# Optimization experiments

Measured on AMD Instinct MI355X. Metric: run time of the kernel, lower is better.

The kernel has to match this reference:

```python
import jax, jax.numpy as jnp
import numpy as np

EPS_POS = 0.65
EPS_NEG = 0.4
TAU = 0.03
TEMPERATURE = 0.07


def setup_inputs() -> dict:
    key = jax.random.key(0)
    k1, k2 = jax.random.split(key)
    N, H, W, C = 256, 14, 14, 512  # ResNet18 layer4 features (448x448 frame), pooled audio
    frame = jax.random.normal(k1, (N, H, W, C), dtype=jnp.float32)
    audio = jax.random.normal(k2, (N, C), dtype=jnp.float32)
    return {"frame": frame, "audio": audio}


def reference(frame, audio):
    # frame: [N, H, W, C] vision backbone features; audio: [N, C] pooled audio embedding
    N = frame.shape[0]
    f = frame * jax.lax.rsqrt(jnp.sum(frame * frame, axis=3, keepdims=True))  # l2_normalize axis=3
    a = audio * jax.lax.rsqrt(jnp.sum(audio * audio, axis=1, keepdims=True))  # l2_normalize axis=1

    # S_ii: per-sample spatial similarity map [N, 1, H, W]
    S_ii = jnp.einsum('nhwc,nc->nhw', f, a)[:, None, :, :]
    # S_ij: cross-batch similarity [N, K, H, W] (K == N)
    S_ij = jnp.einsum('nhwc,kc->nkhw', f, a)

    m_ip = jax.nn.sigmoid((S_ii - EPS_POS) / TAU)   # positive soft-mask
    neg = 1.0 - jax.nn.sigmoid((S_ii - EPS_NEG) / TAU)  # hard-negative soft-mask

    # Pi: masked mean of positive similarities -> [N, 1]
    Pi = jnp.sum(m_ip * S_ii, axis=(2, 3)) / jnp.sum(m_ip, axis=(2, 3))

    n_all = jax.nn.sigmoid((S_ij - EPS_POS) / TAU)
    mask = 1.0 - 100.0 * jnp.eye(N, dtype=frame.dtype)  # kill diagonal (self) pairs
    Ni_easy = (jnp.sum(n_all * S_ij, axis=(2, 3)) / jnp.sum(n_all, axis=(2, 3))) * mask  # [N, N]
    Ni_hard = jnp.sum(neg * S_ii, axis=(2, 3)) / jnp.sum(neg, axis=(2, 3))  # [N, 1]

    data = jnp.concatenate([Pi, Ni_hard, Ni_easy], axis=1) * TEMPERATURE  # [N, N+2]

    # __calc_loss (faithful to TF broadcasting: Pi_d is [N,1], Ni_d is [N] -> [N,N] broadcast)
    Pi_d = data[:, 0:1]
    Ni_d = jnp.sum(data[:, 1:], axis=1)
    Pi_e = jnp.exp(Pi_d)
    Ni_e = jnp.exp(Ni_d)
    loss = (-1.0 / N) * jnp.sum(jnp.log(Pi_e / (Pi_e + Ni_e)))
    return loss
```

## Files before the change

kernel.cpp:

```cpp
#include <hip/hip_runtime.h>
#include <stdint.h>

#define NFR 256
#define HW 196
#define CH 512
#define EPS_POS 0.65f
#define EPS_NEG 0.40f
#define INV_TAU (1.0f/0.03f)
#define TEMP 0.07f

typedef __bf16 bf16x8 __attribute__((ext_vector_type(8)));
typedef float f32x4 __attribute__((ext_vector_type(4)));

typedef const __attribute__((address_space(1))) unsigned int* as1_u32p;
typedef __attribute__((address_space(3))) unsigned int* as3_u32p;
#define GLL(gp, lp) __builtin_amdgcn_global_load_lds((as1_u32p)(const void*)(gp), (as3_u32p)(void*)(lp), 16, 0, 0)

__device__ __forceinline__ float sigmoidf_(float x) {
  return 1.0f / (1.0f + __expf(-x));
}

__device__ __forceinline__ unsigned short f2bf(float x) {
  unsigned int u = __float_as_uint(x);
  unsigned int r = u + 0x7FFFu + ((u >> 16) & 1u);
  return (unsigned short)(r >> 16);
}

__global__ __launch_bounds__(64) void audio_norm_k(const float* __restrict__ audio,
                                                   unsigned short* __restrict__ abf) {
  const int r = blockIdx.x;
  const int l = threadIdx.x;
  const float4* src = reinterpret_cast<const float4*>(audio + (size_t)r * CH);
  float4 a = src[l];
  float4 b = src[64 + l];
  float ss = a.x*a.x + a.y*a.y + a.z*a.z + a.w*a.w
           + b.x*b.x + b.y*b.y + b.z*b.z + b.w*b.w;
#pragma unroll
  for (int m = 1; m < 64; m <<= 1) ss += __shfl_xor(ss, m);
  float sc = rsqrtf(ss);
  ushort4 o;
  o.x = f2bf(a.x*sc); o.y = f2bf(a.y*sc); o.z = f2bf(a.z*sc); o.w = f2bf(a.w*sc);
  reinterpret_cast<ushort4*>(abf + (size_t)r * CH)[l] = o;
  o.x = f2bf(b.x*sc); o.y = f2bf(b.y*sc); o.z = f2bf(b.z*sc); o.w = f2bf(b.w*sc);
  reinterpret_cast<ushort4*>(abf + (size_t)r * CH)[64 + l] = o;
}

__global__ __launch_bounds__(256) void frame_norm_k(const float* __restrict__ frame,
                                                    unsigned short* __restrict__ fbf) {
  const int w = threadIdx.x >> 6;
  const int l = threadIdx.x & 63;
  const size_t r = (size_t)blockIdx.x * 4 + w;
  const float4* src = reinterpret_cast<const float4*>(frame + r * CH);
  float4 a = src[l];
  float4 b = src[64 + l];
  float ss = a.x*a.x + a.y*a.y + a.z*a.z + a.w*a.w
           + b.x*b.x + b.y*b.y + b.z*b.z + b.w*b.w;
#pragma unroll
  for (int m = 1; m < 64; m <<= 1) ss += __shfl_xor(ss, m);
  float sc = rsqrtf(ss);
  ushort4 o;
  o.x = f2bf(a.x*sc); o.y = f2bf(a.y*sc); o.z = f2bf(a.z*sc); o.w = f2bf(a.w*sc);
  reinterpret_cast<ushort4*>(fbf + r * CH)[l] = o;
  o.x = f2bf(b.x*sc); o.y = f2bf(b.y*sc); o.z = f2bf(b.z*sc); o.w = f2bf(b.w*sc);
  reinterpret_cast<ushort4*>(fbf + r * CH)[64 + l] = o;
}

__global__ __launch_bounds__(256, 3) void simk(const unsigned short* __restrict__ fbf,
                                               const unsigned short* __restrict__ abf,
                                               float* __restrict__ num, float* __restrict__ den,
                                               float* __restrict__ negnum, float* __restrict__ negden) {
  __shared__ unsigned short Alds[2][64][32];
  __shared__ unsigned short Blds[2][256][32];
  const int tid = threadIdx.x;
  const int l = tid & 63, w = tid >> 6;
  const int m0 = blockIdx.x * 64;

  const int scol = (((l & 3) ^ ((l >> 3) & 3)) * 8);
  const unsigned short* agA = fbf + (size_t)(m0 + 16 * w + (l >> 2)) * CH + scol;
  const unsigned short* agB = abf + (size_t)(64 * w + (l >> 2)) * CH + scol;

  GLL(agA, &Alds[0][16 * w][0]);
#pragma unroll
  for (int q = 0; q < 4; ++q)
    GLL(agB + (size_t)(16 * q) * CH, &Blds[0][64 * w + 16 * q][0]);
  __syncthreads();

  f32x4 acc[4][4] = {};
  const int rA = l & 15;
  const int cswz = (((l >> 4) ^ ((l >> 1) & 3)) << 4);
  int buf = 0;

  for (int t = 0; t < 16; ++t) {
    if (t < 15) {
      const int ko = (t + 1) * 32;
      GLL(agA + ko, &Alds[buf ^ 1][16 * w][0]);
#pragma unroll
      for (int q = 0; q < 4; ++q)
        GLL(agB + ko + (size_t)(16 * q) * CH, &Blds[buf ^ 1][64 * w + 16 * q][0]);
    }
    const char* Ab = (const char*)&Alds[buf][0][0] + rA * 64 + cswz;
    const char* Bb = (const char*)&Blds[buf][0][0] + (64 * w + rA) * 64 + cswz;
    bf16x8 af[4], bfr[4];
#pragma unroll
    for (int i = 0; i < 4; ++i) {
      af[i]  = *reinterpret_cast<const bf16x8*>(Ab + 1024 * i);
      bfr[i] = *reinterpret_cast<const bf16x8*>(Bb + 1024 * i);
    }
#pragma unroll
    for (int i = 0; i < 4; ++i)
#pragma unroll
      for (int j = 0; j < 4; ++j)
        acc[i][j] = __builtin_amdgcn_mfma_f32_16x16x32_bf16(af[i], bfr[j], acc[i][j], 0, 0, 0);
    __syncthreads();
    buf ^= 1;
  }

  const int rg = l >> 4;
  const int colL = l & 15;
  const int nlo = m0 / HW;
  const int nhi = (m0 + 63) / HW;

  float cn0[4] = {}, cd0[4] = {}, cn1[4] = {}, cd1[4] = {};
  float gn0 = 0.f, gd0 = 0.f, gn1 = 0.f, gd1 = 0.f;
#pragma unroll
  for (int i = 0; i < 4; ++i) {
#pragma unroll
    for (int jj = 0; jj < 4; ++jj) {
      const int P = m0 + i * 16 + rg * 4 + jj;
      const int nrow = P / HW;
      const bool lo = (nrow == nlo);
#pragma unroll
      for (int j = 0; j < 4; ++j) {
        const float s = acc[i][j][jj];
        const float wp = sigmoidf_((s - EPS_POS) * INV_TAU);
        const float wps = wp * s;
        if (lo) { cn0[j] += wps; cd0[j] += wp; }
        else    { cn1[j] += wps; cd1[j] += wp; }
        const int kglob = w * 64 + j * 16 + colL;
        if (kglob == nrow) {
          const float wneg = 1.f - sigmoidf_((s - EPS_NEG) * INV_TAU);
          if (lo) { gn0 += wneg * s; gd0 += wneg; }
          else    { gn1 += wneg * s; gd1 += wneg; }
        }
      }
    }
  }
  if (gd0 > 0.f) { atomicAdd(&negnum[nlo], gn0); atomicAdd(&negden[nlo], gd0); }
  if (gd1 > 0.f) { atomicAdd(&negnum[nhi], gn1); atomicAdd(&negden[nhi], gd1); }

#pragma unroll
  for (int j = 0; j < 4; ++j) {
    float v0 = cn0[j], d0 = cd0[j], v1 = cn1[j], d1 = cd1[j];
    v0 += __shfl_xor(v0, 16); v0 += __shfl_xor(v0, 32);
    d0 += __shfl_xor(d0, 16); d0 += __shfl_xor(d0, 32);
    v1 += __shfl_xor(v1, 16); v1 += __shfl_xor(v1, 32);
    d1 += __shfl_xor(d1, 16); d1 += __shfl_xor(d1, 32);
    if (rg == 0) {
      const int kglob = w * 64 + j * 16 + colL;
      atomicAdd(&num[nlo * NFR + kglob], v0);
      atomicAdd(&den[nlo * NFR + kglob], d0);
      if (nhi != nlo) {
        atomicAdd(&num[nhi * NFR + kglob], v1);
        atomicAdd(&den[nhi * NFR + kglob], d1);
      }
    }
  }
}

__global__ __launch_bounds__(64) void rowstats_k(const float* __restrict__ num,
                                                 const float* __restrict__ den,
                                                 const float* __restrict__ negnum,
                                                 const float* __restrict__ negden,
                                                 float* __restrict__ Pi_d,
                                                 float* __restrict__ Ni_d) {
  const int r = blockIdx.x;
  const int l = threadIdx.x;
  float vsum = 0.f, pvac = 0.f;
#pragma unroll
  for (int cb = 0; cb < 4; ++cb) {
    const int k = cb * 64 + l;
    const float ratio = num[r * NFR + k] / den[r * NFR + k];
    vsum += ratio;
    if (k == r) pvac = ratio;
  }
#pragma unroll
  for (int m = 1; m < 64; m <<= 1) {
    vsum += __shfl_xor(vsum, m);
    pvac += __shfl_xor(pvac, m);
  }
  if (l == 0) {
    const float nh = negnum[r] / negden[r];
    Pi_d[r] = TEMP * pvac;
    Ni_d[r] = TEMP * (nh + vsum - 100.f * pvac);
  }
}

__global__ __launch_bounds__(256) void loss_k(const float* __restrict__ Pi_d,
                                              const float* __restrict__ Ni_d,
                                              float* __restrict__ out) {
  __shared__ float red[4];
  const int i = blockIdx.x;
  const int tid = threadIdx.x;
  const int l = tid & 63, w = tid >> 6;
  const float x = Ni_d[tid] - Pi_d[i];
  const float m = fmaxf(x, 0.f);
  float sp = m + __logf(__expf(x - m) + __expf(-m));
#pragma unroll
  for (int s2 = 1; s2 < 64; s2 <<= 1) sp += __shfl_xor(sp, s2);
  if (l == 0) red[w] = sp;
  __syncthreads();
  if (tid == 0) atomicAdd(out, (red[0] + red[1] + red[2] + red[3]) * (1.0f / (float)NFR));
}

extern "C" void kernel_launch(void* const* d_in, const int* in_sizes, int n_in,
                              void* d_out, int out_size, void* d_ws, size_t ws_size,
                              hipStream_t stream) {
  const float* frame = (const float*)d_in[0];
  const float* audio = (const float*)d_in[1];
  float* out = (float*)d_out;

  char* ws = (char*)d_ws;
  unsigned short* abf = (unsigned short*)ws;
  unsigned short* fbf = (unsigned short*)(ws + 262144);
  float* num    = (float*)(ws + 262144 + 51380224);
  float* den    = num + NFR * NFR;
  float* negnum = den + NFR * NFR;
  float* negden = negnum + NFR;
  float* Pi_d   = negden + NFR;
  float* Ni_d   = Pi_d + NFR;

  hipMemsetAsync(num, 0, (size_t)(2 * NFR * NFR + 2 * NFR) * sizeof(float), stream);
  hipMemsetAsync(out, 0, sizeof(float), stream);

  audio_norm_k<<<256, 64, 0, stream>>>(audio, abf);
  frame_norm_k<<<12544, 256, 0, stream>>>(frame, fbf);
  simk<<<784, 256, 0, stream>>>(fbf, abf, num, den, negnum, negden);
  rowstats_k<<<256, 64, 0, stream>>>(num, den, negnum, negden, Pi_d, Ni_d);
  loss_k<<<256, 256, 0, stream>>>(Pi_d, Ni_d, out);
}
```

Measured before the change: 202.6 us.

## Fuse frame normalization into similarity GEMM and fold memsets into kernels

The separate frame normalization kernel is removed. The GEMM kernel now reads fp32 frame rows directly, L2-normalizes them, converts them to bf16 and keeps the full 64x512 A tile in swizzled LDS. This avoids writing and re-reading a ~51MB bf16 intermediate. The two memsets are replaced by zeroing inside audio_norm_k and rowstats_k, which saves launches. In exchange, the B operand loses double buffering and now uses an extra barrier per K step, and the larger LDS footprint drops occupancy to 2 blocks.

```diff
diff --git a/kernel.cpp b/kernel.cpp
--- a/kernel.cpp
+++ b/kernel.cpp
@@ -11,6 +11,7 @@
 
 typedef __bf16 bf16x8 __attribute__((ext_vector_type(8)));
 typedef float f32x4 __attribute__((ext_vector_type(4)));
+typedef unsigned short u16x8 __attribute__((ext_vector_type(8)));
 
 typedef const __attribute__((address_space(1))) unsigned int* as1_u32p;
 typedef __attribute__((address_space(3))) unsigned int* as3_u32p;
@@ -27,9 +28,19 @@
 }
 
 __global__ __launch_bounds__(64) void audio_norm_k(const float* __restrict__ audio,
-                                                   unsigned short* __restrict__ abf) {
+                                                   unsigned short* __restrict__ abf,
+                                                   float* __restrict__ numbase,
+                                                   float* __restrict__ negbase) {
   const int r = blockIdx.x;
   const int l = threadIdx.x;
+  {
+    const int idx = r * 64 + l;
+    f32x4 z = {0.f, 0.f, 0.f, 0.f};
+    f32x4* p = (f32x4*)numbase;
+    p[idx * 2] = z;
+    p[idx * 2 + 1] = z;
+    if (r < 2) ((f32x4*)negbase)[r * 64 + l] = z;
+  }
   const float4* src = reinterpret_cast<const float4*>(audio + (size_t)r * CH);
   float4 a = src[l];
   float4 b = src[64 + l];
@@ -45,65 +56,58 @@
   reinterpret_cast<ushort4*>(abf + (size_t)r * CH)[64 + l] = o;
 }
 
-__global__ __launch_bounds__(256) void frame_norm_k(const float* __restrict__ frame,
-                                                    unsigned short* __restrict__ fbf) {
-  const int w = threadIdx.x >> 6;
-  const int l = threadIdx.x & 63;
-  const size_t r = (size_t)blockIdx.x * 4 + w;
-  const float4* src = reinterpret_cast<const float4*>(frame + r * CH);
-  float4 a = src[l];
-  float4 b = src[64 + l];
-  float ss = a.x*a.x + a.y*a.y + a.z*a.z + a.w*a.w
-           + b.x*b.x + b.y*b.y + b.z*b.z + b.w*b.w;
-#pragma unroll
-  for (int m = 1; m < 64; m <<= 1) ss += __shfl_xor(ss, m);
-  float sc = rsqrtf(ss);
-  ushort4 o;
-  o.x = f2bf(a.x*sc); o.y = f2bf(a.y*sc); o.z = f2bf(a.z*sc); o.w = f2bf(a.w*sc);
-  reinterpret_cast<ushort4*>(fbf + r * CH)[l] = o;
-  o.x = f2bf(b.x*sc); o.y = f2bf(b.y*sc); o.z = f2bf(b.z*sc); o.w = f2bf(b.w*sc);
-  reinterpret_cast<ushort4*>(fbf + r * CH)[64 + l] = o;
-}
-
-__global__ __launch_bounds__(256, 3) void simk(const unsigned short* __restrict__ fbf,
+__global__ __launch_bounds__(256, 2) void simk(const float* __restrict__ frame,
                                                const unsigned short* __restrict__ abf,
                                                float* __restrict__ num, float* __restrict__ den,
                                                float* __restrict__ negnum, float* __restrict__ negden) {
-  __shared__ unsigned short Alds[2][64][32];
-  __shared__ unsigned short Blds[2][256][32];
+  __shared__ unsigned short Afull[64][512];
+  __shared__ unsigned short Blds[256][32];
   const int tid = threadIdx.x;
   const int l = tid & 63, w = tid >> 6;
   const int m0 = blockIdx.x * 64;
 
-  const int scol = (((l & 3) ^ ((l >> 3) & 3)) * 8);
-  const unsigned short* agA = fbf + (size_t)(m0 + 16 * w + (l >> 2)) * CH + scol;
-  const unsigned short* agB = abf + (size_t)(64 * w + (l >> 2)) * CH + scol;
-
-  GLL(agA, &Alds[0][16 * w][0]);
+  const int scolB = (((l & 3) ^ ((l >> 3) & 3)) * 8);
+  const unsigned short* agB = abf + (size_t)(64 * w + (l >> 2)) * CH + scolB;
+
 #pragma unroll
   for (int q = 0; q < 4; ++q)
-    GLL(agB + (size_t)(16 * q) * CH, &Blds[0][64 * w + 16 * q][0]);
+    GLL(agB + (size_t)(16 * q) * CH, &Blds[64 * w + 16 * q][0]);
+
+  {
+    const int l8 = l * 8;
+#pragma unroll 2
+    for (int rr = 0; rr < 16; ++rr) {
+      const int r = 16 * w + rr;
+      const float4* src = reinterpret_cast<const float4*>(frame + (size_t)(m0 + r) * CH + l8);
+      float4 a = src[0];
+      float4 b = src[1];
+      float ss = a.x*a.x + a.y*a.y + a.z*a.z + a.w*a.w
+               + b.x*b.x + b.y*b.y + b.z*b.z + b.w*b.w;
+#pragma unroll
+      for (int m = 1; m < 64; m <<= 1) ss += __shfl_xor(ss, m);
+      const float sc = rsqrtf(ss);
+      u16x8 o;
+      o[0] = f2bf(a.x*sc); o[1] = f2bf(a.y*sc); o[2] = f2bf(a.z*sc); o[3] = f2bf(a.w*sc);
+      o[4] = f2bf(b.x*sc); o[5] = f2bf(b.y*sc); o[6] = f2bf(b.z*sc); o[7] = f2bf(b.w*sc);
+      char* dst = (char*)&Afull[0][0] + r * 1024 + ((l ^ (r & 7)) << 4);
+      *reinterpret_cast<u16x8*>(dst) = o;
+    }
+  }
   __syncthreads();
 
   f32x4 acc[4][4] = {};
   const int rA = l & 15;
-  const int cswz = (((l >> 4) ^ ((l >> 1) & 3)) << 4);
-  int buf = 0;
+  const int aRowByte = rA * 1024;
+  const int cswzB = (((l >> 4) ^ ((l >> 1) & 3)) << 4);
 
   for (int t = 0; t < 16; ++t) {
-    if (t < 15) {
-      const int ko = (t + 1) * 32;
-      GLL(agA + ko, &Alds[buf ^ 1][16 * w][0]);
-#pragma unroll
-      for (int q = 0; q < 4; ++q)
-        GLL(agB + ko + (size_t)(16 * q) * CH, &Blds[buf ^ 1][64 * w + 16 * q][0]);
-    }
-    const char* Ab = (const char*)&Alds[buf][0][0] + rA * 64 + cswz;
-    const char* Bb = (const char*)&Blds[buf][0][0] + (64 * w + rA) * 64 + cswz;
+    const int gA = (((4 * t + (l >> 4)) ^ (l & 7)) << 4);
+    const char* Ab = (const char*)&Afull[0][0] + aRowByte + gA;
+    const char* Bb = (const char*)&Blds[0][0] + (64 * w + rA) * 64 + cswzB;
     bf16x8 af[4], bfr[4];
 #pragma unroll
     for (int i = 0; i < 4; ++i) {
-      af[i]  = *reinterpret_cast<const bf16x8*>(Ab + 1024 * i);
+      af[i]  = *reinterpret_cast<const bf16x8*>(Ab + 16384 * i);
       bfr[i] = *reinterpret_cast<const bf16x8*>(Bb + 1024 * i);
     }
 #pragma unroll
@@ -112,7 +116,13 @@
       for (int j = 0; j < 4; ++j)
         acc[i][j] = __builtin_amdgcn_mfma_f32_16x16x32_bf16(af[i], bfr[j], acc[i][j], 0, 0, 0);
     __syncthreads();
-    buf ^= 1;
+    if (t < 15) {
+      const unsigned short* bsrc = agB + (t + 1) * 32;
+#pragma unroll
+      for (int q = 0; q < 4; ++q)
+        GLL(bsrc + (size_t)(16 * q) * CH, &Blds[64 * w + 16 * q][0]);
+      __syncthreads();
+    }
   }
 
   const int rg = l >> 4;
@@ -172,9 +182,11 @@
                                                  const float* __restrict__ negnum,
                                                  const float* __restrict__ negden,
                                                  float* __restrict__ Pi_d,
-                                                 float* __restrict__ Ni_d) {
+                                                 float* __restrict__ Ni_d,
+                                                 float* __restrict__ out) {
   const int r = blockIdx.x;
   const int l = threadIdx.x;
+  if (r == 0 && l == 0) out[0] = 0.f;
   float vsum = 0.f, pvac = 0.f;
 #pragma unroll
   for (int cb = 0; cb < 4; ++cb) {
@@ -221,20 +233,15 @@
 
   char* ws = (char*)d_ws;
   unsigned short* abf = (unsigned short*)ws;
-  unsigned short* fbf = (unsigned short*)(ws + 262144);
-  float* num    = (float*)(ws + 262144 + 51380224);
+  float* num    = (float*)(ws + 262144);
   float* den    = num + NFR * NFR;
   float* negnum = den + NFR * NFR;
   float* negden = negnum + NFR;
   float* Pi_d   = negden + NFR;
   float* Ni_d   = Pi_d + NFR;
 
-  hipMemsetAsync(num, 0, (size_t)(2 * NFR * NFR + 2 * NFR) * sizeof(float), stream);
-  hipMemsetAsync(out, 0, sizeof(float), stream);
-
-  audio_norm_k<<<256, 64, 0, stream>>>(audio, abf);
-  frame_norm_k<<<12544, 256, 0, stream>>>(frame, fbf);
-  simk<<<784, 256, 0, stream>>>(fbf, abf, num, den, negnum, negden);
-  rowstats_k<<<256, 64, 0, stream>>>(num, den, negnum, negden, Pi_d, Ni_d);
+  audio_norm_k<<<256, 64, 0, stream>>>(audio, abf, num, negnum);
+  simk<<<784, 256, 0, stream>>>(frame, abf, num, den, negnum, negden);
+  rowstats_k<<<256, 64, 0, stream>>>(num, den, negnum, negden, Pi_d, Ni_d, out);
   loss_k<<<256, 256, 0, stream>>>(Pi_d, Ni_d, out);
 }
```

New measurement: 189.1 us. 6.6% less time.
